# Performance work log

Measured on AMD Instinct MI355X. Metric: run time of the kernel, lower is better.

## Reference

```python
import jax, jax.numpy as jnp
import numpy as np

N_WIRES = 12
N_QLAYERS = 2
DIM = 2 ** N_WIRES


def setup_inputs() -> dict:
    key = jax.random.key(0)
    k0, k1, k2, k3 = jax.random.split(key, 4)
    x = jax.random.normal(k0, (2048, 1024), dtype=jnp.float32)
    # TT cores: ranks [1,16,1], input dims [32,32], output dims [8,9]
    core0 = jax.random.normal(k1, (1, 32, 8, 16), dtype=jnp.float32) * 0.05
    core1 = jax.random.normal(k2, (16, 32, 9, 1), dtype=jnp.float32) * 0.05
    tt_bias = jnp.zeros((72,), dtype=jnp.float32)
    global_angles = jax.random.normal(k3, (N_QLAYERS, N_WIRES, 3), dtype=jnp.float32) * 0.1
    return {"x": x, "core0": core0, "core1": core1, "tt_bias": tt_bias,
            "global_angles": global_angles}


def _rot(angles):
    # angles [..., 3] -> combined U = Rz @ Ry @ Rx, shape [..., 2, 2] complex64
    half = angles * 0.5
    cx, sx = jnp.cos(half[..., 0]), jnp.sin(half[..., 0])
    cy, sy = jnp.cos(half[..., 1]), jnp.sin(half[..., 1])
    cz, sz = jnp.cos(half[..., 2]), jnp.sin(half[..., 2])
    zero = jnp.zeros_like(cx)
    cplx = jax.lax.complex
    Rx = jnp.stack([jnp.stack([cplx(cx, zero), cplx(zero, -sx)], -1),
                    jnp.stack([cplx(zero, -sx), cplx(cx, zero)], -1)], -2)
    Ry = jnp.stack([jnp.stack([cplx(cy, zero), cplx(-sy, zero)], -1),
                    jnp.stack([cplx(sy, zero), cplx(cy, zero)], -1)], -2)
    ez, ezc = cplx(cz, -sz), cplx(cz, sz)  # exp(-i z/2), exp(+i z/2)
    zc = cplx(zero, zero)
    Rz = jnp.stack([jnp.stack([ez, zc], -1), jnp.stack([zc, ezc], -1)], -2)
    return jnp.einsum('...ij,...jk,...kl->...il', Rz, Ry, Rx)


def _apply_1q(state, U, w):
    # state [bsz, 2^n]; U [bsz, 2, 2]; wire 0 = most significant qubit
    bsz = state.shape[0]
    left, right = 2 ** w, 2 ** (N_WIRES - w - 1)
    s = state.reshape(bsz, left, 2, right)
    s = jnp.einsum('bij,bljr->blir', U, s)
    return s.reshape(bsz, DIM)


def _cnot(state, c, t):
    bsz = state.shape[0]
    s = state.reshape((bsz,) + (2,) * N_WIRES)
    s0 = jax.lax.index_in_dim(s, 0, c + 1, keepdims=True)
    s1 = jax.lax.index_in_dim(s, 1, c + 1, keepdims=True)
    s1 = jnp.flip(s1, axis=t + 1)  # flip target amplitudes where control = 1
    return jnp.concatenate([s0, s1], axis=c + 1).reshape(bsz, DIM)


def reference(x, core0, core1, tt_bias, global_angles):
    bsz = x.shape[0]
    # --- TT layer: x[b,32,32] contracted with two TT cores -> [b,8,9] -> [b,72]
    x_rs = x.reshape(bsz, 32, 32)
    tt_out = jnp.einsum('bij,aipq,qjrs->bpr', x_rs, core0, core1).reshape(bsz, -1) + tt_bias
    # residual global angles
    angles = global_angles[None, :, :, :] + tt_out.reshape(bsz, N_QLAYERS, N_WIRES, 3)
    U = _rot(angles)  # [bsz, L, n, 2, 2]
    # --- tensor-product Ry encoding of x[:, :n_wires] on |0...0>
    enc = x[:, :N_WIRES] * 0.5
    amp = jnp.stack([jnp.cos(enc), jnp.sin(enc)], -1)  # [bsz, n, 2]
    state = amp[:, 0, :]
    for w in range(1, N_WIRES):
        state = (state[:, :, None] * amp[:, w, None, :]).reshape(bsz, -1)
    state = state.astype(jnp.complex64)  # [bsz, 2^n]
    # --- VQC layers: fused Rz@Ry@Rx per wire, then ring CNOT (noise_prob=0)
    for k in range(N_QLAYERS):
        for w in range(N_WIRES):
            state = _apply_1q(state, U[:, k, w], w)
        for i in range(N_WIRES - 1):
            state = _cnot(state, i, i + 1)
        state = _cnot(state, N_WIRES - 1, 0)
    # --- MeasureAll(PauliZ): <Z_w> per wire
    probs = jnp.real(state * jnp.conj(state))  # [bsz, 2^n]
    idx = jnp.arange(DIM)[:, None]
    bits = (idx >> jnp.arange(N_WIRES - 1, -1, -1)[None, :]) & 1  # [2^n, n]
    zsign = (1.0 - 2.0 * bits).astype(jnp.float32)
    return probs @ zsign  # [bsz, n_wires]
```

## Files before the change

### kernel.cpp

```cpp
#include <hip/hip_runtime.h>
#include <math.h>

#define N_WIRES 12

__host__ __device__ constexpr int parity12(int x) {
  x ^= x >> 8; x ^= x >> 4; x ^= x >> 2; x ^= x >> 1;
  return x & 1;
}

typedef float2 f2;
__device__ __forceinline__ f2 mk2(float a, float b) { f2 r; r.x = a; r.y = b; return r; }
__device__ __forceinline__ f2 pkmul(f2 a, f2 b) {
  f2 d; asm("v_pk_mul_f32 %0, %1, %2" : "=v"(d) : "v"(a), "v"(b)); return d;
}
__device__ __forceinline__ f2 pkfma(f2 a, f2 b, f2 c) {
  f2 d; asm("v_pk_fma_f32 %0, %1, %2, %3" : "=v"(d) : "v"(a), "v"(b), "v"(c)); return d;
}
__device__ __forceinline__ f2 shfl_xor2(f2 v, int m) {
  f2 r; r.x = __shfl_xor(v.x, m, 64); r.y = __shfl_xor(v.y, m, 64); return r;
}
__device__ __forceinline__ f2 swap2(f2 v) { return mk2(v.y, v.x); }

struct cpx { float r, i; };
__device__ __forceinline__ cpx cmulc(cpx a, cpx b) {
  return {a.r * b.r - a.i * b.i, a.r * b.i + a.i * b.r};
}

__global__ __launch_bounds__(256) void build_w_kernel(
    const float* __restrict__ core0,
    const float* __restrict__ core1,
    float* __restrict__ Wt) {
  int idx = blockIdx.x * 256 + threadIdx.x;
  int k = idx / 72;
  int o = idx - k * 72;
  int i = k >> 5, jj = k & 31;
  int p = o / 9, r = o - p * 9;
  float acc = 0.f;
#pragma unroll
  for (int q = 0; q < 16; ++q) {
    acc += core0[(i * 8 + p) * 16 + q] * core1[(q * 32 + jj) * 9 + r];
  }
  int og = o / 9, j = o - og * 9;
  Wt[k * 96 + og * 12 + j] = acc;
}

__global__ __launch_bounds__(512) void tt_gemm2(
    const float* __restrict__ x,
    const float* __restrict__ Wt,
    const float* __restrict__ bias,
    float* __restrict__ ttout) {
  __shared__ __align__(16) float ws[128 * 96];
  __shared__ __align__(16) float xs[8 * 132];
  __shared__ float part[16 * 8 * 73];
  const int t = threadIdx.x;
  const int row0 = blockIdx.x * 8;
  const int kk = t >> 5;
  const int rp = (t >> 3) & 3;
  const int og = t & 7;
  const int r0 = rp * 2;

  float a0[9], a1[9];
#pragma unroll
  for (int j = 0; j < 9; ++j) { a0[j] = 0.f; a1[j] = 0.f; }

  for (int s = 0; s < 8; ++s) {
    __syncthreads();
    const float4* Wg = (const float4*)(Wt + s * 128 * 96);
#pragma unroll
    for (int i = 0; i < 6; ++i) {
      const int idx = i * 512 + t;
      ((float4*)ws)[idx] = Wg[idx];
    }
    if (t < 256) {
      const int rr = t >> 5, j4 = t & 31;
      *(float4*)&xs[rr * 132 + j4 * 4] =
          *(const float4*)(x + (size_t)(row0 + rr) * 1024 + s * 128 + j4 * 4);
    }
    __syncthreads();
#pragma unroll
    for (int i = 0; i < 8; ++i) {
      const int k = kk + i * 16;
      const float4 wA = *(const float4*)&ws[k * 96 + og * 12];
      const float4 wB = *(const float4*)&ws[k * 96 + og * 12 + 4];
      const float w8 = ws[k * 96 + og * 12 + 8];
      const float x0v = xs[r0 * 132 + k];
      const float x1v = xs[r0 * 132 + 132 + k];
      a0[0] += x0v * wA.x; a0[1] += x0v * wA.y;
      a0[2] += x0v * wA.z; a0[3] += x0v * wA.w;
      a0[4] += x0v * wB.x; a0[5] += x0v * wB.y;
      a0[6] += x0v * wB.z; a0[7] += x0v * wB.w;
      a0[8] += x0v * w8;
      a1[0] += x1v * wA.x; a1[1] += x1v * wA.y;
      a1[2] += x1v * wA.z; a1[3] += x1v * wA.w;
      a1[4] += x1v * wB.x; a1[5] += x1v * wB.y;
      a1[6] += x1v * wB.z; a1[7] += x1v * wB.w;
      a1[8] += x1v * w8;
    }
  }

#pragma unroll
  for (int j = 0; j < 9; ++j) {
    part[(kk * 8 + r0) * 73 + og * 9 + j] = a0[j];
    part[(kk * 8 + r0 + 1) * 73 + og * 9 + j] = a1[j];
  }
  __syncthreads();

  for (int i = t; i < 576; i += 512) {
    const int r = i / 72, o = i - r * 72;
    float ssum = bias[o];
#pragma unroll
    for (int kq = 0; kq < 16; ++kq) ssum += part[(kq * 8 + r) * 73 + o];
    ttout[(size_t)(row0 + r) * 72 + o] = ssum;
  }
}

template <int MASK, int ROW>
__device__ __forceinline__ void gate_pk(f2 R[32], f2 I[32],
    float u00r, float u00i, float u01r, float u01i, int lane) {
  constexpr int RM = MASK & 0x3F;
  constexpr int LM = (MASK >> 6) & 0x3F;
  constexpr int FLIP = parity12(ROW & 3);
  constexpr int JX = (RM == 0) ? 0 : (((RM & 1) ? (RM ^ 3) : RM) >> 1);
  constexpr bool SW = (RM & 1) != 0;

  const int tsgn = (__popc((ROW >> 6) & lane) & 1) << 31;
  const float dEi = __int_as_float(__float_as_int(u00i) ^ tsgn);
  const float oEr = __int_as_float(__float_as_int(u01r) ^ tsgn);
  const float ndEi = -dEi, noEr = -oEr;
  const f2 A  = mk2(u00r, u00r);
  const f2 C  = mk2(u01i, u01i);
  const f2 nC = mk2(-u01i, -u01i);

  auto Dof = [&](int pe, int ph) { return mk2(pe ? ndEi : dEi, ph ? ndEi : dEi); };
  auto Oof = [&](int pe, int ph) { return mk2(pe ? noEr : oEr, ph ? noEr : oEr); };

  auto upd = [&](int j, f2 Rb, f2 Ib, f2& outR, f2& outI) {
    const int pe = parity12(ROW & (2 * j));
    const int ph = pe ^ FLIP;
    const f2 Dj = Dof(pe, ph), nDj = Dof(!pe, !ph), Oj = Oof(pe, ph);
    const f2 a = R[j], ii = I[j];
    outR = pkfma(A, a, pkfma(nDj, ii, pkfma(Oj, Rb, pkmul(nC, Ib))));
    outI = pkfma(Dj, a, pkfma(A, ii, pkfma(C, Rb, pkmul(Oj, Ib))));
  };

  if constexpr (LM != 0 && RM == 0) {
#pragma unroll
    for (int j = 0; j < 32; ++j) {
      const f2 Rb = shfl_xor2(R[j], LM);
      const f2 Ib = shfl_xor2(I[j], LM);
      f2 nR, nI;
      upd(j, Rb, Ib, nR, nI);
      R[j] = nR; I[j] = nI;
    }
  } else if constexpr (LM != 0 && RM != 0) {
#pragma unroll
    for (int j = 0; j < 32; ++j) {
      const int j2 = j ^ JX;
      if (j < j2) {
        f2 Rb1 = shfl_xor2(R[j2], LM), Ib1 = shfl_xor2(I[j2], LM);
        f2 Rb2 = shfl_xor2(R[j],  LM), Ib2 = shfl_xor2(I[j],  LM);
        if constexpr (SW) {
          Rb1 = swap2(Rb1); Ib1 = swap2(Ib1);
          Rb2 = swap2(Rb2); Ib2 = swap2(Ib2);
        }
        f2 nR1, nI1, nR2, nI2;
        upd(j, Rb1, Ib1, nR1, nI1);
        upd(j2, Rb2, Ib2, nR2, nI2);
        R[j] = nR1; I[j] = nI1; R[j2] = nR2; I[j2] = nI2;
      }
    }
  } else {
#pragma unroll
    for (int j = 0; j < 32; ++j) {
      const int j2 = j ^ JX;
      if (j < j2) {
        f2 Rb1 = R[j2], Ib1 = I[j2], Rb2 = R[j], Ib2 = I[j];
        if constexpr (SW) {
          Rb1 = swap2(Rb1); Ib1 = swap2(Ib1);
          Rb2 = swap2(Rb2); Ib2 = swap2(Ib2);
        }
        f2 nR1, nI1, nR2, nI2;
        upd(j, Rb1, Ib1, nR1, nI1);
        upd(j2, Rb2, Ib2, nR2, nI2);
        R[j] = nR1; I[j] = nI1; R[j2] = nR2; I[j2] = nI2;
      }
    }
  }
}

__global__ __launch_bounds__(256, 2) void vqc_kernel6(
    const float* __restrict__ x,
    const float* __restrict__ ttout,
    const float* __restrict__ gang,
    float* __restrict__ out) {
  const int t = threadIdx.x;
  const int lane = t & 63;
  const int b = blockIdx.x * 4 + (t >> 6);
  const float* ttb = ttout + (size_t)b * 72;

  float c0 = 0.f, c1 = 0.f, c2 = 0.f, c3 = 0.f;
  const bool uLane = lane < 12;
  const bool fLane = (lane >= 16) && (lane < 28);
  if (uLane || fLane) {
    const int w = uLane ? lane : lane - 16;
    const int k = uLane ? 1 : 0;
    const int gbase = (k * 12 + w) * 3;
    const int tbase = k * 36 + w * 3;
    const float a0 = gang[gbase + 0] + ttb[tbase + 0];
    const float a1 = gang[gbase + 1] + ttb[tbase + 1];
    const float a2 = gang[gbase + 2] + ttb[tbase + 2];
    const float cx = cosf(0.5f * a0), sx = sinf(0.5f * a0);
    const float cy = cosf(0.5f * a1), sy = sinf(0.5f * a1);
    const float cz = cosf(0.5f * a2), sz = sinf(0.5f * a2);
    const float m00r = cy * cx,   m00i = sy * sx;
    const float m01r = -sy * cx,  m01i = -cy * sx;
    const float m10r = sy * cx,   m10i = -cy * sx;
    const float m11r = cy * cx,   m11i = -sy * sx;
    const float U00r = cz * m00r + sz * m00i, U00i = cz * m00i - sz * m00r;
    const float U01r = cz * m01r + sz * m01i, U01i = cz * m01i - sz * m01r;
    const float U10r = cz * m10r - sz * m10i, U10i = cz * m10i + sz * m10r;
    const float U11r = cz * m11r - sz * m11i, U11i = cz * m11i + sz * m11r;
    if (uLane) {
      c0 = U00r; c1 = U00i; c2 = U01r; c3 = U01i;
    } else {
      const float e = x[(size_t)b * 1024 + w] * 0.5f;
      const float cc = cosf(e), ss = sinf(e);
      c0 = U00r * cc + U01r * ss;  c1 = U00i * cc + U01i * ss;
      c2 = U10r * cc + U11r * ss;  c3 = U10i * cc + U11i * ss;
    }
  }

  const int bwv0 = (lane >> 5) & 1;
  const int bwv1 = ((lane >> 4) ^ (lane >> 3)) & 1;
  const int bwv2 = ((lane >> 3) ^ (lane >> 2)) & 1;
  const int bwv3 = ((lane >> 2) ^ (lane >> 1)) & 1;
  const int bwv4 = ((lane >> 1) ^ lane) & 1;
  const int l0 = lane & 1;

  cpx P;
  {
    const float f0r = __shfl(c0, 16, 64), f0i = __shfl(c1, 16, 64);
    const float f1r = __shfl(c2, 16, 64), f1i = __shfl(c3, 16, 64);
    P = {bwv0 ? f1r : f0r, bwv0 ? f1i : f0i};
  }
  const int bwrest[4] = {bwv1, bwv2, bwv3, bwv4};
#pragma unroll
  for (int w = 1; w < 5; ++w) {
    const float f0r = __shfl(c0, 16 + w, 64), f0i = __shfl(c1, 16 + w, 64);
    const float f1r = __shfl(c2, 16 + w, 64), f1i = __shfl(c3, 16 + w, 64);
    const int bb = bwrest[w - 1];
    P = cmulc(P, {bb ? f1r : f0r, bb ? f1i : f0i});
  }

  cpx PT[8];
  {
    cpx F5a, F5b, F6[2], F7[2];
    {
      const cpx q0 = {__shfl(c0, 21, 64), __shfl(c1, 21, 64)};
      const cpx q1 = {__shfl(c2, 21, 64), __shfl(c3, 21, 64)};
      F5a = l0 ? q1 : q0;
      F5b = l0 ? q0 : q1;
    }
    F6[0] = {__shfl(c0, 22, 64), __shfl(c1, 22, 64)};
    F6[1] = {__shfl(c2, 22, 64), __shfl(c3, 22, 64)};
    F7[0] = {__shfl(c0, 23, 64), __shfl(c1, 23, 64)};
    F7[1] = {__shfl(c2, 23, 64), __shfl(c3, 23, 64)};
    const cpx P5a = cmulc(P, F5a), P5b = cmulc(P, F5b);
    cpx t56[4];
#pragma unroll
    for (int i = 0; i < 4; ++i) {
      const int r5 = i >> 1, r4 = i & 1;
      t56[i] = cmulc(r5 ? P5b : P5a, F6[r5 ^ r4]);
    }
#pragma unroll
    for (int i = 0; i < 8; ++i) {
      const int r4 = (i >> 1) & 1, r3 = i & 1;
      PT[i] = cmulc(t56[i >> 1], F7[r4 ^ r3]);
    }
  }

  cpx TL[16];
  {
    cpx F8[2], F9[2], F10[2], F11[2];
    F8[0]  = {__shfl(c0, 24, 64), __shfl(c1, 24, 64)};
    F8[1]  = {__shfl(c2, 24, 64), __shfl(c3, 24, 64)};
    F9[0]  = {__shfl(c0, 25, 64), __shfl(c1, 25, 64)};
    F9[1]  = {__shfl(c2, 25, 64), __shfl(c3, 25, 64)};
    F10[0] = {__shfl(c0, 26, 64), __shfl(c1, 26, 64)};
    F10[1] = {__shfl(c2, 26, 64), __shfl(c3, 26, 64)};
    F11[0] = {__shfl(c0, 27, 64), __shfl(c1, 27, 64)};
    F11[1] = {__shfl(c2, 27, 64), __shfl(c3, 27, 64)};
    cpx t10[4];
#pragma unroll
    for (int i = 0; i < 4; ++i) {
      const int r1 = i >> 1, r0 = i & 1;
      t10[i] = cmulc(F10[r1 ^ r0], F11[r0]);
    }
    cpx t9[8];
#pragma unroll
    for (int i = 0; i < 8; ++i) {
      const int r2 = i >> 2, r1 = (i >> 1) & 1;
      t9[i] = cmulc(F9[r2 ^ r1], t10[i & 3]);
    }
#pragma unroll
    for (int i = 0; i < 16; ++i) {
      const int r3 = i >> 3, r2 = (i >> 2) & 1;
      TL[i] = cmulc(F8[r3 ^ r2], t9[i & 7]);
    }
  }

  f2 R[32], I[32];
#pragma unroll
  for (int j = 0; j < 32; ++j) {
    const cpx Av = PT[(j >> 2) & 7];
    const int il = (2 * j) & 15;
    const f2 Tre = mk2(TL[il].r, TL[il ^ 3].r);
    const f2 Tim = mk2(TL[il].i, TL[il ^ 3].i);
    const f2 Ar = mk2(Av.r, Av.r);
    R[j] = pkfma(mk2(-Av.i, -Av.i), Tim, pkmul(Ar, Tre));
    I[j] = pkfma(mk2(Av.i, Av.i), Tre, pkmul(Ar, Tim));
  }

#define GATE(MASK, ROW, G)                                                  \
  gate_pk<MASK, ROW>(R, I, __shfl(c0, G, 64), __shfl(c1, G, 64),            \
                     __shfl(c2, G, 64), __shfl(c3, G, 64), lane)

  GATE(0xC00, 0x400, 0);
  GATE(0x200, 0xE00, 1);
  GATE(0x100, 0xD00, 2);
  GATE(0x080, 0xC80, 3);
  GATE(0x040, 0xC40, 4);
  GATE(0x020, 0xC20, 5);
  GATE(0x010, 0xC10, 6);
  GATE(0x008, 0xC08, 7);
  GATE(0x004, 0xC04, 8);
  GATE(0x002, 0xC02, 9);
  GATE(0x001, 0xC01, 10);
  GATE(0xBFF, 0xC00, 11);
#undef GATE

  constexpr int MROWS[12] = {0xFFF, 0xA00, 0x700, 0xB80, 0x7C0, 0xBE0,
                             0x7F0, 0xBF8, 0x7FC, 0xBFE, 0x7FF, 0xBFF};
  const f2 Spp = mk2(1.f, 1.f),  Smm = mk2(-1.f, -1.f);
  const f2 Spm = mk2(1.f, -1.f), Smp = mk2(-1.f, 1.f);
  f2 acc2[12];
#pragma unroll
  for (int w = 0; w < 12; ++w) acc2[w] = mk2(0.f, 0.f);
#pragma unroll
  for (int j = 0; j < 32; ++j) {
    const f2 pr2 = pkfma(I[j], I[j], pkmul(R[j], R[j]));
#pragma unroll
    for (int w = 0; w < 12; ++w) {
      const int sl = parity12(MROWS[w] & (2 * j));
      const int sh = sl ^ parity12(MROWS[w] & 3);
      const f2 S = sl ? (sh ? Smm : Smp) : (sh ? Spm : Spp);
      acc2[w] = pkfma(S, pr2, acc2[w]);
    }
  }
#pragma unroll
  for (int w = 0; w < 12; ++w) {
    float v = acc2[w].x + acc2[w].y;
    if (__popc((MROWS[w] >> 6) & lane) & 1) v = -v;
#pragma unroll
    for (int off = 32; off > 0; off >>= 1) v += __shfl_down(v, off, 64);
    if (lane == 0) out[(size_t)b * 12 + w] = v;
  }
}

extern "C" void kernel_launch(void* const* d_in, const int* in_sizes, int n_in,
                              void* d_out, int out_size, void* d_ws, size_t ws_size,
                              hipStream_t stream) {
  const float* x       = (const float*)d_in[0];
  const float* core0   = (const float*)d_in[1];
  const float* core1   = (const float*)d_in[2];
  const float* tt_bias = (const float*)d_in[3];
  const float* gang    = (const float*)d_in[4];
  float* out = (float*)d_out;
  float* Wt     = (float*)d_ws;
  float* ttout  = (float*)d_ws + 98304;

  const int bsz = in_sizes[0] / 1024;

  build_w_kernel<<<288, 256, 0, stream>>>(core0, core1, Wt);
  tt_gemm2<<<bsz / 8, 512, 0, stream>>>(x, Wt, tt_bias, ttout);
  vqc_kernel6<<<bsz / 4, 256, 0, stream>>>(x, ttout, gang, out);
}
```

Before: 54.12 us.

## Remap qubit-to-lane bits for DPP/swizzle shuffles and read W from global

Permutes which qubit bits map to lane-index bits so that cross-lane gate exchanges use DPP quad permutes, permlane swaps or ds_swizzle instead of generic ds_bpermute-based __shfl_xor. Broadcast of per-wire gate coefficients switches from __shfl to readlane. The TT GEMM stops staging W tiles in LDS and reads W directly from global/L2, cutting LDS traffic and occupancy pressure at the cost of more global loads. The lane remapping changes initial-state construction and sign masks accordingly, which risks correctness if any mapping is wrong.

```diff
diff --git a/kernel.cpp b/kernel.cpp
--- a/kernel.cpp
+++ b/kernel.cpp
@@ -6,6 +6,12 @@
 __host__ __device__ constexpr int parity12(int x) {
   x ^= x >> 8; x ^= x >> 4; x ^= x >> 2; x ^= x >> 1;
   return x & 1;
+}
+
+__host__ __device__ constexpr int lanemask_of(int m) {
+  return (((m >> 9) & 1) << 0) | (((m >> 8) & 1) << 1) |
+         (((m >> 11) & 1) << 2) | (((m >> 10) & 1) << 3) |
+         (((m >> 7) & 1) << 4) | (((m >> 6) & 1) << 5);
 }
 
 typedef float2 f2;
@@ -16,14 +22,51 @@
 __device__ __forceinline__ f2 pkfma(f2 a, f2 b, f2 c) {
   f2 d; asm("v_pk_fma_f32 %0, %1, %2, %3" : "=v"(d) : "v"(a), "v"(b), "v"(c)); return d;
 }
-__device__ __forceinline__ f2 shfl_xor2(f2 v, int m) {
-  f2 r; r.x = __shfl_xor(v.x, m, 64); r.y = __shfl_xor(v.y, m, 64); return r;
-}
 __device__ __forceinline__ f2 swap2(f2 v) { return mk2(v.y, v.x); }
 
 struct cpx { float r, i; };
 __device__ __forceinline__ cpx cmulc(cpx a, cpx b) {
   return {a.r * b.r - a.i * b.i, a.r * b.i + a.i * b.r};
+}
+__device__ __forceinline__ cpx fpick(float r0, float i0, float r1, float i1, int b) {
+  cpx c; c.r = b ? r1 : r0; c.i = b ? i1 : i0; return c;
+}
+__device__ __forceinline__ float rl(float v, int l) {
+  return __int_as_float(__builtin_amdgcn_readlane(__float_as_int(v), l));
+}
+
+template <int LM>
+__device__ __forceinline__ float lshfl(float v, int lane) {
+  if constexpr (LM == 0) {
+    return v;
+  } else if constexpr (LM == 0x01) {
+    return __int_as_float(__builtin_amdgcn_mov_dpp(__float_as_int(v), 0xB1, 0xF, 0xF, true));
+  } else if constexpr (LM == 0x02) {
+    return __int_as_float(__builtin_amdgcn_mov_dpp(__float_as_int(v), 0x4E, 0xF, 0xF, true));
+  } else if constexpr (LM == 0x03) {
+    return __int_as_float(__builtin_amdgcn_mov_dpp(__float_as_int(v), 0x1B, 0xF, 0xF, true));
+  } else if constexpr ((LM & 0x20) != 0) {
+#if __has_builtin(__builtin_amdgcn_permlane32_swap)
+    auto p = __builtin_amdgcn_permlane32_swap(__float_as_int(v), __float_as_int(v), false, false);
+    const float tv = __int_as_float((lane & 32) ? (int)p[0] : (int)p[1]);
+    return lshfl<LM & 0x1F>(tv, lane);
+#else
+    return __shfl_xor(v, LM, 64);
+#endif
+  } else if constexpr (LM == 0x10) {
+#if __has_builtin(__builtin_amdgcn_permlane16_swap)
+    auto p = __builtin_amdgcn_permlane16_swap(__float_as_int(v), __float_as_int(v), false, false);
+    return __int_as_float((lane & 16) ? (int)p[0] : (int)p[1]);
+#else
+    return __int_as_float(__builtin_amdgcn_ds_swizzle(__float_as_int(v), (0x10 << 10) | 0x1F));
+#endif
+  } else {
+    return __int_as_float(__builtin_amdgcn_ds_swizzle(__float_as_int(v), (LM << 10) | 0x1F));
+  }
+}
+template <int LM>
+__device__ __forceinline__ f2 lshfl2(f2 v, int lane) {
+  return mk2(lshfl<LM>(v.x, lane), lshfl<LM>(v.y, lane));
 }
 
 __global__ __launch_bounds__(256) void build_w_kernel(
@@ -44,12 +87,11 @@
   Wt[k * 96 + og * 12 + j] = acc;
 }
 
-__global__ __launch_bounds__(512) void tt_gemm2(
+__global__ __launch_bounds__(512) void tt_gemm3(
     const float* __restrict__ x,
     const float* __restrict__ Wt,
     const float* __restrict__ bias,
     float* __restrict__ ttout) {
-  __shared__ __align__(16) float ws[128 * 96];
   __shared__ __align__(16) float xs[8 * 132];
   __shared__ float part[16 * 8 * 73];
   const int t = threadIdx.x;
@@ -65,24 +107,19 @@
 
   for (int s = 0; s < 8; ++s) {
     __syncthreads();
-    const float4* Wg = (const float4*)(Wt + s * 128 * 96);
-#pragma unroll
-    for (int i = 0; i < 6; ++i) {
-      const int idx = i * 512 + t;
-      ((float4*)ws)[idx] = Wg[idx];
-    }
     if (t < 256) {
       const int rr = t >> 5, j4 = t & 31;
       *(float4*)&xs[rr * 132 + j4 * 4] =
           *(const float4*)(x + (size_t)(row0 + rr) * 1024 + s * 128 + j4 * 4);
     }
     __syncthreads();
+    const float* Wp = Wt + (size_t)s * 128 * 96;
 #pragma unroll
     for (int i = 0; i < 8; ++i) {
       const int k = kk + i * 16;
-      const float4 wA = *(const float4*)&ws[k * 96 + og * 12];
-      const float4 wB = *(const float4*)&ws[k * 96 + og * 12 + 4];
-      const float w8 = ws[k * 96 + og * 12 + 8];
+      const float4 wA = *(const float4*)(Wp + k * 96 + og * 12);
+      const float4 wB = *(const float4*)(Wp + k * 96 + og * 12 + 4);
+      const float w8 = Wp[k * 96 + og * 12 + 8];
       const float x0v = xs[r0 * 132 + k];
       const float x1v = xs[r0 * 132 + 132 + k];
       a0[0] += x0v * wA.x; a0[1] += x0v * wA.y;
@@ -118,12 +155,13 @@
 __device__ __forceinline__ void gate_pk(f2 R[32], f2 I[32],
     float u00r, float u00i, float u01r, float u01i, int lane) {
   constexpr int RM = MASK & 0x3F;
-  constexpr int LM = (MASK >> 6) & 0x3F;
+  constexpr int LMP = lanemask_of(MASK);
+  constexpr int ROWL = lanemask_of(ROW);
   constexpr int FLIP = parity12(ROW & 3);
   constexpr int JX = (RM == 0) ? 0 : (((RM & 1) ? (RM ^ 3) : RM) >> 1);
   constexpr bool SW = (RM & 1) != 0;
 
-  const int tsgn = (__popc((ROW >> 6) & lane) & 1) << 31;
+  const int tsgn = (__popc(ROWL & lane) & 1) << 31;
   const float dEi = __int_as_float(__float_as_int(u00i) ^ tsgn);
   const float oEr = __int_as_float(__float_as_int(u01r) ^ tsgn);
   const float ndEi = -dEi, noEr = -oEr;
@@ -143,22 +181,22 @@
     outI = pkfma(Dj, a, pkfma(A, ii, pkfma(C, Rb, pkmul(Oj, Ib))));
   };
 
-  if constexpr (LM != 0 && RM == 0) {
+  if constexpr (LMP != 0 && RM == 0) {
 #pragma unroll
     for (int j = 0; j < 32; ++j) {
-      const f2 Rb = shfl_xor2(R[j], LM);
-      const f2 Ib = shfl_xor2(I[j], LM);
+      const f2 Rb = lshfl2<LMP>(R[j], lane);
+      const f2 Ib = lshfl2<LMP>(I[j], lane);
       f2 nR, nI;
       upd(j, Rb, Ib, nR, nI);
       R[j] = nR; I[j] = nI;
     }
-  } else if constexpr (LM != 0 && RM != 0) {
+  } else if constexpr (LMP != 0 && RM != 0) {
 #pragma unroll
     for (int j = 0; j < 32; ++j) {
       const int j2 = j ^ JX;
       if (j < j2) {
-        f2 Rb1 = shfl_xor2(R[j2], LM), Ib1 = shfl_xor2(I[j2], LM);
-        f2 Rb2 = shfl_xor2(R[j],  LM), Ib2 = shfl_xor2(I[j],  LM);
+        f2 Rb1 = lshfl2<LMP>(R[j2], lane), Ib1 = lshfl2<LMP>(I[j2], lane);
+        f2 Rb2 = lshfl2<LMP>(R[j],  lane), Ib2 = lshfl2<LMP>(I[j],  lane);
         if constexpr (SW) {
           Rb1 = swap2(Rb1); Ib1 = swap2(Ib1);
           Rb2 = swap2(Rb2); Ib2 = swap2(Ib2);
@@ -188,7 +226,7 @@
   }
 }
 
-__global__ __launch_bounds__(256, 2) void vqc_kernel6(
+__global__ __launch_bounds__(256, 2) void vqc_kernel7(
     const float* __restrict__ x,
     const float* __restrict__ ttout,
     const float* __restrict__ gang,
@@ -230,41 +268,26 @@
     }
   }
 
-  const int bwv0 = (lane >> 5) & 1;
-  const int bwv1 = ((lane >> 4) ^ (lane >> 3)) & 1;
-  const int bwv2 = ((lane >> 3) ^ (lane >> 2)) & 1;
-  const int bwv3 = ((lane >> 2) ^ (lane >> 1)) & 1;
-  const int bwv4 = ((lane >> 1) ^ lane) & 1;
-  const int l0 = lane & 1;
-
-  cpx P;
-  {
-    const float f0r = __shfl(c0, 16, 64), f0i = __shfl(c1, 16, 64);
-    const float f1r = __shfl(c2, 16, 64), f1i = __shfl(c3, 16, 64);
-    P = {bwv0 ? f1r : f0r, bwv0 ? f1i : f0i};
-  }
-  const int bwrest[4] = {bwv1, bwv2, bwv3, bwv4};
-#pragma unroll
-  for (int w = 1; w < 5; ++w) {
-    const float f0r = __shfl(c0, 16 + w, 64), f0i = __shfl(c1, 16 + w, 64);
-    const float f1r = __shfl(c2, 16 + w, 64), f1i = __shfl(c3, 16 + w, 64);
-    const int bb = bwrest[w - 1];
-    P = cmulc(P, {bb ? f1r : f0r, bb ? f1i : f0i});
-  }
+  const int bwv0 = (lane >> 2) & 1;
+  const int bwv1 = ((lane >> 3) ^ lane) & 1;
+  const int bwv2 = (lane ^ (lane >> 1)) & 1;
+  const int bwv3 = ((lane >> 1) ^ (lane >> 4)) & 1;
+  const int bwv4 = ((lane >> 4) ^ (lane >> 5)) & 1;
+  const int l5 = (lane >> 5) & 1;
+
+  cpx P = fpick(rl(c0, 16), rl(c1, 16), rl(c2, 16), rl(c3, 16), bwv0);
+  P = cmulc(P, fpick(rl(c0, 17), rl(c1, 17), rl(c2, 17), rl(c3, 17), bwv1));
+  P = cmulc(P, fpick(rl(c0, 18), rl(c1, 18), rl(c2, 18), rl(c3, 18), bwv2));
+  P = cmulc(P, fpick(rl(c0, 19), rl(c1, 19), rl(c2, 19), rl(c3, 19), bwv3));
+  P = cmulc(P, fpick(rl(c0, 20), rl(c1, 20), rl(c2, 20), rl(c3, 20), bwv4));
 
   cpx PT[8];
   {
-    cpx F5a, F5b, F6[2], F7[2];
-    {
-      const cpx q0 = {__shfl(c0, 21, 64), __shfl(c1, 21, 64)};
-      const cpx q1 = {__shfl(c2, 21, 64), __shfl(c3, 21, 64)};
-      F5a = l0 ? q1 : q0;
-      F5b = l0 ? q0 : q1;
-    }
-    F6[0] = {__shfl(c0, 22, 64), __shfl(c1, 22, 64)};
-    F6[1] = {__shfl(c2, 22, 64), __shfl(c3, 22, 64)};
-    F7[0] = {__shfl(c0, 23, 64), __shfl(c1, 23, 64)};
-    F7[1] = {__shfl(c2, 23, 64), __shfl(c3, 23, 64)};
+    const cpx F5a = fpick(rl(c0, 21), rl(c1, 21), rl(c2, 21), rl(c3, 21), l5);
+    const cpx F5b = fpick(rl(c0, 21), rl(c1, 21), rl(c2, 21), rl(c3, 21), l5 ^ 1);
+    cpx F6[2], F7[2];
+    F6[0] = {rl(c0, 22), rl(c1, 22)};  F6[1] = {rl(c2, 22), rl(c3, 22)};
+    F7[0] = {rl(c0, 23), rl(c1, 23)};  F7[1] = {rl(c2, 23), rl(c3, 23)};
     const cpx P5a = cmulc(P, F5a), P5b = cmulc(P, F5b);
     cpx t56[4];
 #pragma unroll
@@ -282,14 +305,10 @@
   cpx TL[16];
   {
     cpx F8[2], F9[2], F10[2], F11[2];
-    F8[0]  = {__shfl(c0, 24, 64), __shfl(c1, 24, 64)};
-    F8[1]  = {__shfl(c2, 24, 64), __shfl(c3, 24, 64)};
-    F9[0]  = {__shfl(c0, 25, 64), __shfl(c1, 25, 64)};
-    F9[1]  = {__shfl(c2, 25, 64), __shfl(c3, 25, 64)};
-    F10[0] = {__shfl(c0, 26, 64), __shfl(c1, 26, 64)};
-    F10[1] = {__shfl(c2, 26, 64), __shfl(c3, 26, 64)};
-    F11[0] = {__shfl(c0, 27, 64), __shfl(c1, 27, 64)};
-    F11[1] = {__shfl(c2, 27, 64), __shfl(c3, 27, 64)};
+    F8[0]  = {rl(c0, 24), rl(c1, 24)};  F8[1]  = {rl(c2, 24), rl(c3, 24)};
+    F9[0]  = {rl(c0, 25), rl(c1, 25)};  F9[1]  = {rl(c2, 25), rl(c3, 25)};
+    F10[0] = {rl(c0, 26), rl(c1, 26)};  F10[1] = {rl(c2, 26), rl(c3, 26)};
+    F11[0] = {rl(c0, 27), rl(c1, 27)};  F11[1] = {rl(c2, 27), rl(c3, 27)};
     cpx t10[4];
 #pragma unroll
     for (int i = 0; i < 4; ++i) {
@@ -322,8 +341,7 @@
   }
 
 #define GATE(MASK, ROW, G)                                                  \
-  gate_pk<MASK, ROW>(R, I, __shfl(c0, G, 64), __shfl(c1, G, 64),            \
-                     __shfl(c2, G, 64), __shfl(c3, G, 64), lane)
+  gate_pk<MASK, ROW>(R, I, rl(c0, G), rl(c1, G), rl(c2, G), rl(c3, G), lane)
 
   GATE(0xC00, 0x400, 0);
   GATE(0x200, 0xE00, 1);
@@ -360,7 +378,7 @@
 #pragma unroll
   for (int w = 0; w < 12; ++w) {
     float v = acc2[w].x + acc2[w].y;
-    if (__popc((MROWS[w] >> 6) & lane) & 1) v = -v;
+    if (__popc(lanemask_of(MROWS[w]) & lane) & 1) v = -v;
 #pragma unroll
     for (int off = 32; off > 0; off >>= 1) v += __shfl_down(v, off, 64);
     if (lane == 0) out[(size_t)b * 12 + w] = v;
@@ -382,6 +400,6 @@
   const int bsz = in_sizes[0] / 1024;
 
   build_w_kernel<<<288, 256, 0, stream>>>(core0, core1, Wt);
-  tt_gemm2<<<bsz / 8, 512, 0, stream>>>(x, Wt, tt_bias, ttout);
-  vqc_kernel6<<<bsz / 4, 256, 0, stream>>>(x, ttout, gang, out);
-}
+  tt_gemm3<<<bsz / 8, 512, 0, stream>>>(x, Wt, tt_bias, ttout);
+  vqc_kernel7<<<bsz / 4, 256, 0, stream>>>(x, ttout, gang, out);
+}
```

New measurement: 57.07 us. 1.05x slower.
